# Kernel tuning notes

Measured on AMD Instinct MI355X. Metric: run time of the kernel, lower is better.

The kernel has to match this reference:

```python
import jax, jax.numpy as jnp
import numpy as np

H = 1024      # hidden_size
I = 4096      # intermediate_size
E = 8         # num_experts
TOP_K = 2
LB_COEF = 0.01


def setup_inputs() -> dict:
    key = jax.random.key(0)
    ks = jax.random.split(key, 8)
    s_h = 1.0 / np.sqrt(H)
    s_i = 1.0 / np.sqrt(I)
    return {
        "x": jax.random.normal(ks[0], (2, 2048, H), dtype=jnp.float32),
        "Wr": jax.random.normal(ks[1], (H, E), dtype=jnp.float32) * s_h,
        "br": jnp.zeros((E,), dtype=jnp.float32),
        "W1": jax.random.normal(ks[2], (E, H, I), dtype=jnp.float32) * s_h,
        "b1": jnp.zeros((E, I), dtype=jnp.float32),
        "W2": jax.random.normal(ks[3], (E, I, H), dtype=jnp.float32) * s_i,
        "b2": jnp.zeros((E, H), dtype=jnp.float32),
    }


def _moe_forward(x, Wr, br, W1, b1, W2, b2):
    B, S, Hd = x.shape
    x_flat = x.reshape(-1, Hd)                      # [T, H]
    T = x_flat.shape[0]

    # ---- Router: softmax probs, top-k, renormalize ----
    logits = x_flat @ Wr + br                       # [T, E]
    probs = jax.nn.softmax(logits, axis=-1)         # [T, E]
    topk_w, topk_idx = jax.lax.top_k(probs, TOP_K)  # [T, K]
    topk_w = topk_w / jnp.sum(topk_w, axis=-1, keepdims=True)

    # ---- Load-balance aux loss (switch-style) ----
    onehot = jax.nn.one_hot(topk_idx, E, dtype=x.dtype)   # [T, K, E]
    frac_tokens = onehot.mean(axis=(0, 1))                 # [E]
    frac_probs = probs.mean(axis=0)                        # [E]
    aux_loss = E * jnp.sum(frac_tokens * frac_probs) * LB_COEF

    # combine_weights[t, e] = routing weight of expert e for token t (0 if unselected)
    combine = jnp.sum(topk_w[..., None] * onehot, axis=1)  # [T, E]

    # ---- Experts: dense per-expert FFN, weighted combine ----
    out = jnp.zeros_like(x_flat)
    for e in range(E):
        h = jax.nn.gelu(x_flat @ W1[e] + b1[e])            # [T, I]
        y = h @ W2[e] + b2[e]                              # [T, H]
        out = out + y * combine[:, e:e + 1]
    return out.reshape(B, S, Hd), aux_loss


def reference(x, Wr, br, W1, b1, W2, b2):
    return _moe_forward(x, Wr, br, W1, b1, W2, b2)
```

## Files before the change

### kernel.cpp

```cpp
#include <hip/hip_runtime.h>
#include <hip/hip_bf16.h>

#define HD 1024
#define ID 4096
#define NE 8
#define NT 4096
#define NSLOT (NT*2)

typedef __attribute__((ext_vector_type(4))) float f32x4;
typedef __attribute__((ext_vector_type(8))) short bf16x8;
typedef __attribute__((ext_vector_type(4))) unsigned int u32x4;
typedef __attribute__((ext_vector_type(2))) unsigned int u32x2;
typedef unsigned short u16;

__device__ __forceinline__ u16 f2b(float f) {
  __hip_bfloat16 h = __float2bfloat16(f);
  return __builtin_bit_cast(unsigned short, h);
}
__device__ __forceinline__ unsigned int pack2(float a, float b) {
  return (unsigned int)f2b(a) | ((unsigned int)f2b(b) << 16);
}
__device__ __forceinline__ void gload16(const void* g, void* l) {
  __builtin_amdgcn_global_load_lds(
      (const __attribute__((address_space(1))) unsigned int*)g,
      (__attribute__((address_space(3))) unsigned int*)l, 16, 0, 0);
}
__device__ __forceinline__ float gelu_tanh(float v) {
  float c = v + 0.044715f * v * v * v;
  return 0.5f * v * (1.0f + tanhf(0.7978845608028654f * c));
}

__global__ __launch_bounds__(256) void k_transpose_bf16(
    const float* __restrict__ src, u16* __restrict__ dst, int R, int C) {
  __shared__ float tile[64][65];
  int e = blockIdx.z;
  int c0 = blockIdx.x * 64;
  int r0 = blockIdx.y * 64;
  int t = threadIdx.x;
  const float* s = src + (size_t)e * R * C;
#pragma unroll
  for (int i = 0; i < 16; ++i) {
    int r = i * 4 + (t >> 6);
    tile[r][t & 63] = s[(size_t)(r0 + r) * C + c0 + (t & 63)];
  }
  __syncthreads();
  u16* d = dst + (size_t)e * R * C;
#pragma unroll
  for (int i = 0; i < 4; ++i) {
    int c = i * 16 + (t >> 4);
    int rb = (t & 15) * 4;
    u32x2 p;
    p[0] = pack2(tile[rb + 0][c], tile[rb + 1][c]);
    p[1] = pack2(tile[rb + 2][c], tile[rb + 3][c]);
    *(u32x2*)&d[(size_t)(c0 + c) * R + r0 + rb] = p;
  }
}

__global__ __launch_bounds__(256) void k_router(
    const float* __restrict__ x, const float* __restrict__ Wr,
    const float* __restrict__ br, int* __restrict__ cnt,
    int* __restrict__ slotE, int* __restrict__ slotLoc,
    float* __restrict__ slotW, float* __restrict__ psumG,
    u16* __restrict__ xb) {
  __shared__ float wrt[NE * HD];
  __shared__ float blkp[NE];
  int t = threadIdx.x;
  if (t < NE) blkp[t] = 0.0f;
  for (int i = t; i < NE * HD; i += 256) wrt[(i & 7) * HD + (i >> 3)] = Wr[i];
  __syncthreads();
  int wave = t >> 6, lane = t & 63;
  int token = blockIdx.x * 4 + wave;
  const float* xr = x + (size_t)token * HD;
  u16* xbr = xb + (size_t)token * HD;
  float acc[NE] = {0, 0, 0, 0, 0, 0, 0, 0};
#pragma unroll 4
  for (int j = 0; j < 16; ++j) {
    int h = j * 64 + lane;
    float xv = xr[h];
    xbr[h] = f2b(xv);
#pragma unroll
    for (int e = 0; e < NE; ++e) acc[e] += xv * wrt[e * HD + h];
  }
#pragma unroll
  for (int d = 1; d < 64; d <<= 1) {
#pragma unroll
    for (int e = 0; e < NE; ++e) acc[e] += __shfl_xor(acc[e], d, 64);
  }
  if (lane == 0) {
    float lg[NE], p[NE];
    float m = -1e30f;
#pragma unroll
    for (int e = 0; e < NE; ++e) { lg[e] = acc[e] + br[e]; m = fmaxf(m, lg[e]); }
    float s = 0.f;
#pragma unroll
    for (int e = 0; e < NE; ++e) { p[e] = expf(lg[e] - m); s += p[e]; }
    float inv = 1.0f / s;
    int i1 = 0, i2 = -1;
    float v1 = -1.f, v2 = -1.f;
#pragma unroll
    for (int e = 0; e < NE; ++e) {
      p[e] *= inv;
      atomicAdd(&blkp[e], p[e]);
      if (p[e] > v1) { v2 = v1; i2 = i1; v1 = p[e]; i1 = e; }
      else if (p[e] > v2) { v2 = p[e]; i2 = e; }
    }
    float wsum = v1 + v2;
    int l1 = atomicAdd(&cnt[i1], 1);
    int l2 = atomicAdd(&cnt[i2], 1);
    slotE[token * 2] = i1;     slotLoc[token * 2] = l1;     slotW[token * 2] = v1 / wsum;
    slotE[token * 2 + 1] = i2; slotLoc[token * 2 + 1] = l2; slotW[token * 2 + 1] = v2 / wsum;
  }
  __syncthreads();
  if (t < NE) atomicAdd(&psumG[t], blkp[t]);
}

__global__ void k_finalize(const float* __restrict__ psumG, const int* __restrict__ cnt,
                           int* __restrict__ off, float* __restrict__ out_aux) {
  if (threadIdx.x == 0) {
    int o = 0;
    float a = 0.f;
    for (int e = 0; e < NE; ++e) {
      off[e] = o;
      o += cnt[e];
      a += ((float)cnt[e] / (float)NSLOT) * (psumG[e] / (float)NT);
    }
    off[NE] = o;
    out_aux[0] = (float)NE * a * 0.01f;
  }
}

__global__ void k_scatter(const int* __restrict__ slotE, const int* __restrict__ slotLoc,
                          const float* __restrict__ slotW, const int* __restrict__ off,
                          int* __restrict__ rowTok, float* __restrict__ rowW) {
  int i = blockIdx.x * 256 + threadIdx.x;
  int pos = off[slotE[i]] + slotLoc[i];
  if (pos < 0) pos = 0;
  if (pos >= NSLOT) pos = NSLOT - 1;
  rowTok[pos] = i >> 1;
  rowW[pos] = slotW[i];
}

#define STG(bf) do { \
    gload16(srcA0, &As[bf][c0 * 8]); \
    gload16(srcA1, &As[bf][c1 * 8]); \
    gload16(srcB0, &Bs[bf][c0 * 8]); \
    gload16(srcB1, &Bs[bf][c1 * 8]); \
    srcA0 += 32; srcA1 += 32; srcB0 += 32; srcB1 += 32; \
  } while (0)

__global__ __launch_bounds__(512, 1) void k_gemm1(
    const u16* __restrict__ xb, const u16* __restrict__ w1t,
    const float* __restrict__ b1, u16* __restrict__ hbuf,
    const int* __restrict__ cnt, const int* __restrict__ off,
    const int* __restrict__ rowTok) {
  int bid = blockIdx.x;
  int e = bid >> 8;
  int m0 = ((bid >> 4) & 15) * 256;
  int n0 = (bid & 15) * 256;
  int ce = cnt[e];
  if (m0 >= ce) return;
  int oe = off[e];
  __shared__ u16 As[3][256 * 32];
  __shared__ u16 Bs[3][256 * 32];
  __shared__ int rtok[256];
  int t = threadIdx.x;
  if (t < 256) {
    int r = m0 + t;
    if (r >= ce) r = ce - 1;
    int tok = rowTok[oe + r];
    rtok[t] = (tok < 0) ? 0 : (tok >= NT ? NT - 1 : tok);
  }
  __syncthreads();
  int c0 = t, c1 = t + 512;
  int js0 = (c0 & 3) ^ ((c0 >> 3) & 3);
  int js1 = (c1 & 3) ^ ((c1 >> 3) & 3);
  const u16* srcA0 = xb + (size_t)rtok[c0 >> 2] * HD + js0 * 8;
  const u16* srcA1 = xb + (size_t)rtok[c1 >> 2] * HD + js1 * 8;
  const u16* bb = w1t + (size_t)e * ID * HD + (size_t)n0 * HD;
  const u16* srcB0 = bb + (size_t)(c0 >> 2) * HD + js0 * 8;
  const u16* srcB1 = bb + (size_t)(c1 >> 2) * HD + js1 * 8;
  int lane = t & 63, wave = t >> 6;
  int wr = wave >> 2, wc = wave & 3;
  f32x4 acc[8][4] = {};
  const int NK = HD / 32;
  STG(0);
  STG(1);
  int rb = 0;
  for (int kt = 0; kt < NK; ++kt) {
    if (kt + 1 < NK) asm volatile("s_waitcnt vmcnt(4)" ::: "memory");
    else             asm volatile("s_waitcnt vmcnt(0)" ::: "memory");
    __builtin_amdgcn_s_barrier();
    bf16x8 af[8], bv[4];
#pragma unroll
    for (int mm = 0; mm < 8; ++mm) {
      int ra = wr * 128 + mm * 16 + (lane & 15);
      int slot = (lane >> 4) ^ ((ra >> 1) & 3);
      af[mm] = *(const bf16x8*)&As[rb][ra * 32 + slot * 8];
    }
#pragma unroll
    for (int nn = 0; nn < 4; ++nn) {
      int rbr = wc * 64 + nn * 16 + (lane & 15);
      int slot = (lane >> 4) ^ ((rbr >> 1) & 3);
      bv[nn] = *(const bf16x8*)&Bs[rb][rbr * 32 + slot * 8];
    }
#pragma unroll
    for (int mm = 0; mm < 8; ++mm)
#pragma unroll
      for (int nn = 0; nn < 4; ++nn)
        acc[mm][nn] = __builtin_amdgcn_mfma_f32_16x16x32_bf16(af[mm], bv[nn], acc[mm][nn], 0, 0, 0);
    if (kt + 2 < NK) {
      int sb = rb + 2; if (sb >= 3) sb -= 3;
      STG(sb);
    }
    rb = (rb == 2) ? 0 : rb + 1;
  }
  const float* b1e = b1 + (size_t)e * ID + n0;
#pragma unroll
  for (int nn = 0; nn < 4; ++nn) {
    int col = wc * 64 + nn * 16 + (lane & 15);
    float bias = b1e[col];
#pragma unroll
    for (int mm = 0; mm < 8; ++mm) {
      int lr0 = wr * 128 + mm * 16 + (lane >> 4) * 4;
#pragma unroll
      for (int r = 0; r < 4; ++r) {
        int grow = m0 + lr0 + r;
        if (grow < ce) {
          float v = acc[mm][nn][r] + bias;
          hbuf[(size_t)(oe + grow) * ID + n0 + col] = f2b(gelu_tanh(v));
        }
      }
    }
  }
}

__global__ __launch_bounds__(512, 1) void k_gemm2(
    const u16* __restrict__ hbuf, const u16* __restrict__ w2t,
    const float* __restrict__ b2, float* __restrict__ out,
    const int* __restrict__ cnt, const int* __restrict__ off,
    const int* __restrict__ rowTok, const float* __restrict__ rowW) {
  int bid = blockIdx.x;
  int e = bid >> 7;
  int m0 = ((bid >> 3) & 15) * 256;
  int n0 = ((bid >> 1) & 3) * 256;
  int ks = bid & 1;
  int ce = cnt[e];
  if (m0 >= ce) return;
  int oe = off[e];
  int k0 = ks * (ID / 2);
  __shared__ u16 As[3][256 * 32];
  __shared__ u16 Bs[3][256 * 32];
  __shared__ int rtok[256];
  __shared__ float rw[256];
  int t = threadIdx.x;
  if (t < 256) {
    int r = m0 + t;
    int rc = (r < ce) ? r : ce - 1;
    int tok = rowTok[oe + rc];
    rtok[t] = (tok < 0) ? 0 : (tok >= NT ? NT - 1 : tok);
    rw[t] = (r < ce) ? rowW[oe + r] : 0.0f;
  }
  __syncthreads();
  int c0 = t, c1 = t + 512;
  int js0 = (c0 & 3) ^ ((c0 >> 3) & 3);
  int js1 = (c1 & 3) ^ ((c1 >> 3) & 3);
  int rA0 = m0 + (c0 >> 2); if (rA0 >= ce) rA0 = ce - 1;
  int rA1 = m0 + (c1 >> 2); if (rA1 >= ce) rA1 = ce - 1;
  const u16* srcA0 = hbuf + (size_t)(oe + rA0) * ID + k0 + js0 * 8;
  const u16* srcA1 = hbuf + (size_t)(oe + rA1) * ID + k0 + js1 * 8;
  const u16* bb = w2t + (size_t)e * HD * ID + (size_t)n0 * ID + k0;
  const u16* srcB0 = bb + (size_t)(c0 >> 2) * ID + js0 * 8;
  const u16* srcB1 = bb + (size_t)(c1 >> 2) * ID + js1 * 8;
  int lane = t & 63, wave = t >> 6;
  int wr = wave >> 2, wc = wave & 3;
  f32x4 acc[8][4] = {};
  const int NK = (ID / 2) / 32;
  STG(0);
  STG(1);
  int rb = 0;
  for (int kt = 0; kt < NK; ++kt) {
    if (kt + 1 < NK) asm volatile("s_waitcnt vmcnt(4)" ::: "memory");
    else             asm volatile("s_waitcnt vmcnt(0)" ::: "memory");
    __builtin_amdgcn_s_barrier();
    bf16x8 af[8], bv[4];
#pragma unroll
    for (int mm = 0; mm < 8; ++mm) {
      int ra = wr * 128 + mm * 16 + (lane & 15);
      int slot = (lane >> 4) ^ ((ra >> 1) & 3);
      af[mm] = *(const bf16x8*)&As[rb][ra * 32 + slot * 8];
    }
#pragma unroll
    for (int nn = 0; nn < 4; ++nn) {
      int rbr = wc * 64 + nn * 16 + (lane & 15);
      int slot = (lane >> 4) ^ ((rbr >> 1) & 3);
      bv[nn] = *(const bf16x8*)&Bs[rb][rbr * 32 + slot * 8];
    }
#pragma unroll
    for (int mm = 0; mm < 8; ++mm)
#pragma unroll
      for (int nn = 0; nn < 4; ++nn)
        acc[mm][nn] = __builtin_amdgcn_mfma_f32_16x16x32_bf16(af[mm], bv[nn], acc[mm][nn], 0, 0, 0);
    if (kt + 2 < NK) {
      int sb = rb + 2; if (sb >= 3) sb -= 3;
      STG(sb);
    }
    rb = (rb == 2) ? 0 : rb + 1;
  }
  const float* b2e = b2 + (size_t)e * HD + n0;
#pragma unroll
  for (int nn = 0; nn < 4; ++nn) {
    int col = wc * 64 + nn * 16 + (lane & 15);
    float bias = (ks == 0) ? b2e[col] : 0.0f;
#pragma unroll
    for (int mm = 0; mm < 8; ++mm) {
      int lr0 = wr * 128 + mm * 16 + (lane >> 4) * 4;
#pragma unroll
      for (int r = 0; r < 4; ++r) {
        int lr = lr0 + r;
        int grow = m0 + lr;
        if (grow < ce) {
          float v = (acc[mm][nn][r] + bias) * rw[lr];
          atomicAdd(&out[(size_t)rtok[lr] * HD + n0 + col], v);
        }
      }
    }
  }
}

extern "C" void kernel_launch(void* const* d_in, const int* in_sizes, int n_in,
                              void* d_out, int out_size, void* d_ws, size_t ws_size,
                              hipStream_t stream) {
  const float* x  = (const float*)d_in[0];
  const float* Wr = (const float*)d_in[1];
  const float* br = (const float*)d_in[2];
  const float* W1 = (const float*)d_in[3];
  const float* b1 = (const float*)d_in[4];
  const float* W2 = (const float*)d_in[5];
  const float* b2 = (const float*)d_in[6];
  float* out = (float*)d_out;

  char* ws = (char*)d_ws;
  size_t o = 0;
  auto alloc = [&](size_t bytes) {
    void* p = ws + o;
    o = (o + bytes + 255) & ~(size_t)255;
    return p;
  };
  u16* xb    = (u16*)alloc((size_t)NT * HD * 2);
  u16* w1t   = (u16*)alloc((size_t)NE * ID * HD * 2);
  u16* w2t   = (u16*)alloc((size_t)NE * ID * HD * 2);
  u16* hbuf  = (u16*)alloc((size_t)NSLOT * ID * 2);
  int* cnt     = (int*)alloc(NE * 4);
  float* psumG = (float*)alloc(NE * 4);
  int* off     = (int*)alloc(16 * 4);
  int* slotE   = (int*)alloc(NSLOT * 4);
  int* slotLoc = (int*)alloc(NSLOT * 4);
  float* slotW = (float*)alloc(NSLOT * 4);
  int* rowTok  = (int*)alloc(NSLOT * 4);
  float* rowW  = (float*)alloc(NSLOT * 4);

  if (ws_size < o) return;

  hipMemsetAsync(cnt, 0, NE * 4, stream);
  hipMemsetAsync(psumG, 0, NE * 4, stream);
  hipMemsetAsync(out, 0, (size_t)out_size * 4, stream);
  k_transpose_bf16<<<dim3(ID / 64, HD / 64, NE), 256, 0, stream>>>(W1, w1t, HD, ID);
  k_transpose_bf16<<<dim3(HD / 64, ID / 64, NE), 256, 0, stream>>>(W2, w2t, ID, HD);
  k_router<<<NT / 4, 256, 0, stream>>>(x, Wr, br, cnt, slotE, slotLoc, slotW, psumG, xb);
  k_finalize<<<1, 64, 0, stream>>>(psumG, cnt, off, out + (size_t)NT * HD);
  k_scatter<<<NSLOT / 256, 256, 0, stream>>>(slotE, slotLoc, slotW, off, rowTok, rowW);
  k_gemm1<<<NE * 16 * 16, 512, 0, stream>>>(xb, w1t, b1, hbuf, cnt, off, rowTok);
  k_gemm2<<<NE * 16 * 4 * 2, 512, 0, stream>>>(hbuf, w2t, b2, out, cnt, off, rowTok, rowW);
}
```

Before: 559.8 us.

## Retile expert GEMMs to 128x256 tiles with 256-thread blocks, two per CU

Both grouped expert GEMMs move from 256x256 tiles run by 512 threads to 128x256 tiles run by 256 threads, with launch bounds allowing two blocks per CU. Each wave now computes 64x128 instead of 128x64, and the staging macro issues six async loads per stage instead of four, with the vmcnt wait adjusted to match. The smaller M tile is meant to waste less work on padded rows at the ragged end of each expert's token count and to give more blocks for load balance. In exchange, each loaded B tile is reused across fewer rows, raising weight traffic, and two resident blocks per CU put more pressure on LDS and registers.

```diff
diff --git a/kernel.cpp b/kernel.cpp
--- a/kernel.cpp
+++ b/kernel.cpp
@@ -141,72 +141,78 @@
 }
 
 #define STG(bf) do { \
-    gload16(srcA0, &As[bf][c0 * 8]); \
-    gload16(srcA1, &As[bf][c1 * 8]); \
-    gload16(srcB0, &Bs[bf][c0 * 8]); \
-    gload16(srcB1, &Bs[bf][c1 * 8]); \
-    srcA0 += 32; srcA1 += 32; srcB0 += 32; srcB1 += 32; \
+    gload16(srcA0, &As[bf][cA0 * 8]); \
+    gload16(srcA1, &As[bf][cA1 * 8]); \
+    gload16(srcB0, &Bs[bf][cB0 * 8]); \
+    gload16(srcB1, &Bs[bf][cB1 * 8]); \
+    gload16(srcB2, &Bs[bf][cB2 * 8]); \
+    gload16(srcB3, &Bs[bf][cB3 * 8]); \
+    srcA0 += 32; srcA1 += 32; srcB0 += 32; srcB1 += 32; srcB2 += 32; srcB3 += 32; \
   } while (0)
 
-__global__ __launch_bounds__(512, 1) void k_gemm1(
+__global__ __launch_bounds__(256, 2) void k_gemm1(
     const u16* __restrict__ xb, const u16* __restrict__ w1t,
     const float* __restrict__ b1, u16* __restrict__ hbuf,
     const int* __restrict__ cnt, const int* __restrict__ off,
     const int* __restrict__ rowTok) {
   int bid = blockIdx.x;
-  int e = bid >> 8;
-  int m0 = ((bid >> 4) & 15) * 256;
+  int e = bid >> 9;
+  int m0 = ((bid >> 4) & 31) * 128;
   int n0 = (bid & 15) * 256;
   int ce = cnt[e];
   if (m0 >= ce) return;
   int oe = off[e];
-  __shared__ u16 As[3][256 * 32];
+  __shared__ u16 As[3][128 * 32];
   __shared__ u16 Bs[3][256 * 32];
-  __shared__ int rtok[256];
+  __shared__ int rtok[128];
   int t = threadIdx.x;
-  if (t < 256) {
+  if (t < 128) {
     int r = m0 + t;
     if (r >= ce) r = ce - 1;
     int tok = rowTok[oe + r];
     rtok[t] = (tok < 0) ? 0 : (tok >= NT ? NT - 1 : tok);
   }
   __syncthreads();
-  int c0 = t, c1 = t + 512;
-  int js0 = (c0 & 3) ^ ((c0 >> 3) & 3);
-  int js1 = (c1 & 3) ^ ((c1 >> 3) & 3);
-  const u16* srcA0 = xb + (size_t)rtok[c0 >> 2] * HD + js0 * 8;
-  const u16* srcA1 = xb + (size_t)rtok[c1 >> 2] * HD + js1 * 8;
+  int cA0 = t, cA1 = t + 256;
+  int cB0 = t, cB1 = t + 256, cB2 = t + 512, cB3 = t + 768;
+  int jA0 = (cA0 & 3) ^ ((cA0 >> 3) & 3), jA1 = (cA1 & 3) ^ ((cA1 >> 3) & 3);
+  int jB0 = (cB0 & 3) ^ ((cB0 >> 3) & 3), jB1 = (cB1 & 3) ^ ((cB1 >> 3) & 3);
+  int jB2 = (cB2 & 3) ^ ((cB2 >> 3) & 3), jB3 = (cB3 & 3) ^ ((cB3 >> 3) & 3);
+  const u16* srcA0 = xb + (size_t)rtok[cA0 >> 2] * HD + jA0 * 8;
+  const u16* srcA1 = xb + (size_t)rtok[cA1 >> 2] * HD + jA1 * 8;
   const u16* bb = w1t + (size_t)e * ID * HD + (size_t)n0 * HD;
-  const u16* srcB0 = bb + (size_t)(c0 >> 2) * HD + js0 * 8;
-  const u16* srcB1 = bb + (size_t)(c1 >> 2) * HD + js1 * 8;
+  const u16* srcB0 = bb + (size_t)(cB0 >> 2) * HD + jB0 * 8;
+  const u16* srcB1 = bb + (size_t)(cB1 >> 2) * HD + jB1 * 8;
+  const u16* srcB2 = bb + (size_t)(cB2 >> 2) * HD + jB2 * 8;
+  const u16* srcB3 = bb + (size_t)(cB3 >> 2) * HD + jB3 * 8;
   int lane = t & 63, wave = t >> 6;
-  int wr = wave >> 2, wc = wave & 3;
-  f32x4 acc[8][4] = {};
+  int wr = wave >> 1, wc = wave & 1;
+  f32x4 acc[4][8] = {};
   const int NK = HD / 32;
   STG(0);
   STG(1);
   int rb = 0;
   for (int kt = 0; kt < NK; ++kt) {
-    if (kt + 1 < NK) asm volatile("s_waitcnt vmcnt(4)" ::: "memory");
+    if (kt + 1 < NK) asm volatile("s_waitcnt vmcnt(6)" ::: "memory");
     else             asm volatile("s_waitcnt vmcnt(0)" ::: "memory");
     __builtin_amdgcn_s_barrier();
-    bf16x8 af[8], bv[4];
-#pragma unroll
-    for (int mm = 0; mm < 8; ++mm) {
-      int ra = wr * 128 + mm * 16 + (lane & 15);
+    bf16x8 af[4], bv[8];
+#pragma unroll
+    for (int mm = 0; mm < 4; ++mm) {
+      int ra = wr * 64 + mm * 16 + (lane & 15);
       int slot = (lane >> 4) ^ ((ra >> 1) & 3);
       af[mm] = *(const bf16x8*)&As[rb][ra * 32 + slot * 8];
     }
 #pragma unroll
-    for (int nn = 0; nn < 4; ++nn) {
-      int rbr = wc * 64 + nn * 16 + (lane & 15);
+    for (int nn = 0; nn < 8; ++nn) {
+      int rbr = wc * 128 + nn * 16 + (lane & 15);
       int slot = (lane >> 4) ^ ((rbr >> 1) & 3);
       bv[nn] = *(const bf16x8*)&Bs[rb][rbr * 32 + slot * 8];
     }
 #pragma unroll
-    for (int mm = 0; mm < 8; ++mm)
-#pragma unroll
-      for (int nn = 0; nn < 4; ++nn)
+    for (int mm = 0; mm < 4; ++mm)
+#pragma unroll
+      for (int nn = 0; nn < 8; ++nn)
         acc[mm][nn] = __builtin_amdgcn_mfma_f32_16x16x32_bf16(af[mm], bv[nn], acc[mm][nn], 0, 0, 0);
     if (kt + 2 < NK) {
       int sb = rb + 2; if (sb >= 3) sb -= 3;
@@ -216,12 +222,12 @@
   }
   const float* b1e = b1 + (size_t)e * ID + n0;
 #pragma unroll
-  for (int nn = 0; nn < 4; ++nn) {
-    int col = wc * 64 + nn * 16 + (lane & 15);
+  for (int nn = 0; nn < 8; ++nn) {
+    int col = wc * 128 + nn * 16 + (lane & 15);
     float bias = b1e[col];
 #pragma unroll
-    for (int mm = 0; mm < 8; ++mm) {
-      int lr0 = wr * 128 + mm * 16 + (lane >> 4) * 4;
+    for (int mm = 0; mm < 4; ++mm) {
+      int lr0 = wr * 64 + mm * 16 + (lane >> 4) * 4;
 #pragma unroll
       for (int r = 0; r < 4; ++r) {
         int grow = m0 + lr0 + r;
@@ -234,26 +240,26 @@
   }
 }
 
-__global__ __launch_bounds__(512, 1) void k_gemm2(
+__global__ __launch_bounds__(256, 2) void k_gemm2(
     const u16* __restrict__ hbuf, const u16* __restrict__ w2t,
     const float* __restrict__ b2, float* __restrict__ out,
     const int* __restrict__ cnt, const int* __restrict__ off,
     const int* __restrict__ rowTok, const float* __restrict__ rowW) {
   int bid = blockIdx.x;
-  int e = bid >> 7;
-  int m0 = ((bid >> 3) & 15) * 256;
+  int e = bid >> 8;
+  int m0 = ((bid >> 3) & 31) * 128;
   int n0 = ((bid >> 1) & 3) * 256;
   int ks = bid & 1;
   int ce = cnt[e];
   if (m0 >= ce) return;
   int oe = off[e];
   int k0 = ks * (ID / 2);
-  __shared__ u16 As[3][256 * 32];
+  __shared__ u16 As[3][128 * 32];
   __shared__ u16 Bs[3][256 * 32];
-  __shared__ int rtok[256];
-  __shared__ float rw[256];
+  __shared__ int rtok[128];
+  __shared__ float rw[128];
   int t = threadIdx.x;
-  if (t < 256) {
+  if (t < 128) {
     int r = m0 + t;
     int rc = (r < ce) ? r : ce - 1;
     int tok = rowTok[oe + rc];
@@ -261,44 +267,48 @@
     rw[t] = (r < ce) ? rowW[oe + r] : 0.0f;
   }
   __syncthreads();
-  int c0 = t, c1 = t + 512;
-  int js0 = (c0 & 3) ^ ((c0 >> 3) & 3);
-  int js1 = (c1 & 3) ^ ((c1 >> 3) & 3);
-  int rA0 = m0 + (c0 >> 2); if (rA0 >= ce) rA0 = ce - 1;
-  int rA1 = m0 + (c1 >> 2); if (rA1 >= ce) rA1 = ce - 1;
-  const u16* srcA0 = hbuf + (size_t)(oe + rA0) * ID + k0 + js0 * 8;
-  const u16* srcA1 = hbuf + (size_t)(oe + rA1) * ID + k0 + js1 * 8;
+  int cA0 = t, cA1 = t + 256;
+  int cB0 = t, cB1 = t + 256, cB2 = t + 512, cB3 = t + 768;
+  int jA0 = (cA0 & 3) ^ ((cA0 >> 3) & 3), jA1 = (cA1 & 3) ^ ((cA1 >> 3) & 3);
+  int jB0 = (cB0 & 3) ^ ((cB0 >> 3) & 3), jB1 = (cB1 & 3) ^ ((cB1 >> 3) & 3);
+  int jB2 = (cB2 & 3) ^ ((cB2 >> 3) & 3), jB3 = (cB3 & 3) ^ ((cB3 >> 3) & 3);
+  int rA0 = m0 + (cA0 >> 2); if (rA0 >= ce) rA0 = ce - 1;
+  int rA1 = m0 + (cA1 >> 2); if (rA1 >= ce) rA1 = ce - 1;
+  const u16* srcA0 = hbuf + (size_t)(oe + rA0) * ID + k0 + jA0 * 8;
+  const u16* srcA1 = hbuf + (size_t)(oe + rA1) * ID + k0 + jA1 * 8;
   const u16* bb = w2t + (size_t)e * HD * ID + (size_t)n0 * ID + k0;
-  const u16* srcB0 = bb + (size_t)(c0 >> 2) * ID + js0 * 8;
-  const u16* srcB1 = bb + (size_t)(c1 >> 2) * ID + js1 * 8;
+  const u16* srcB0 = bb + (size_t)(cB0 >> 2) * ID + jB0 * 8;
+  const u16* srcB1 = bb + (size_t)(cB1 >> 2) * ID + jB1 * 8;
+  const u16* srcB2 = bb + (size_t)(cB2 >> 2) * ID + jB2 * 8;
+  const u16* srcB3 = bb + (size_t)(cB3 >> 2) * ID + jB3 * 8;
   int lane = t & 63, wave = t >> 6;
-  int wr = wave >> 2, wc = wave & 3;
-  f32x4 acc[8][4] = {};
+  int wr = wave >> 1, wc = wave & 1;
+  f32x4 acc[4][8] = {};
   const int NK = (ID / 2) / 32;
   STG(0);
   STG(1);
   int rb = 0;
   for (int kt = 0; kt < NK; ++kt) {
-    if (kt + 1 < NK) asm volatile("s_waitcnt vmcnt(4)" ::: "memory");
+    if (kt + 1 < NK) asm volatile("s_waitcnt vmcnt(6)" ::: "memory");
     else             asm volatile("s_waitcnt vmcnt(0)" ::: "memory");
     __builtin_amdgcn_s_barrier();
-    bf16x8 af[8], bv[4];
-#pragma unroll
-    for (int mm = 0; mm < 8; ++mm) {
-      int ra = wr * 128 + mm * 16 + (lane & 15);
+    bf16x8 af[4], bv[8];
+#pragma unroll
+    for (int mm = 0; mm < 4; ++mm) {
+      int ra = wr * 64 + mm * 16 + (lane & 15);
       int slot = (lane >> 4) ^ ((ra >> 1) & 3);
       af[mm] = *(const bf16x8*)&As[rb][ra * 32 + slot * 8];
     }
 #pragma unroll
-    for (int nn = 0; nn < 4; ++nn) {
-      int rbr = wc * 64 + nn * 16 + (lane & 15);
+    for (int nn = 0; nn < 8; ++nn) {
+      int rbr = wc * 128 + nn * 16 + (lane & 15);
       int slot = (lane >> 4) ^ ((rbr >> 1) & 3);
       bv[nn] = *(const bf16x8*)&Bs[rb][rbr * 32 + slot * 8];
     }
 #pragma unroll
-    for (int mm = 0; mm < 8; ++mm)
-#pragma unroll
-      for (int nn = 0; nn < 4; ++nn)
+    for (int mm = 0; mm < 4; ++mm)
+#pragma unroll
+      for (int nn = 0; nn < 8; ++nn)
         acc[mm][nn] = __builtin_amdgcn_mfma_f32_16x16x32_bf16(af[mm], bv[nn], acc[mm][nn], 0, 0, 0);
     if (kt + 2 < NK) {
       int sb = rb + 2; if (sb >= 3) sb -= 3;
@@ -308,12 +318,12 @@
   }
   const float* b2e = b2 + (size_t)e * HD + n0;
 #pragma unroll
-  for (int nn = 0; nn < 4; ++nn) {
-    int col = wc * 64 + nn * 16 + (lane & 15);
+  for (int nn = 0; nn < 8; ++nn) {
+    int col = wc * 128 + nn * 16 + (lane & 15);
     float bias = (ks == 0) ? b2e[col] : 0.0f;
 #pragma unroll
-    for (int mm = 0; mm < 8; ++mm) {
-      int lr0 = wr * 128 + mm * 16 + (lane >> 4) * 4;
+    for (int mm = 0; mm < 4; ++mm) {
+      int lr0 = wr * 64 + mm * 16 + (lane >> 4) * 4;
 #pragma unroll
       for (int r = 0; r < 4; ++r) {
         int lr = lr0 + r;
@@ -369,6 +379,6 @@
   k_router<<<NT / 4, 256, 0, stream>>>(x, Wr, br, cnt, slotE, slotLoc, slotW, psumG, xb);
   k_finalize<<<1, 64, 0, stream>>>(psumG, cnt, off, out + (size_t)NT * HD);
   k_scatter<<<NSLOT / 256, 256, 0, stream>>>(slotE, slotLoc, slotW, off, rowTok, rowW);
-  k_gemm1<<<NE * 16 * 16, 512, 0, stream>>>(xb, w1t, b1, hbuf, cnt, off, rowTok);
-  k_gemm2<<<NE * 16 * 4 * 2, 512, 0, stream>>>(hbuf, w2t, b2, out, cnt, off, rowTok, rowW);
-}
+  k_gemm1<<<NE * 32 * 16, 256, 0, stream>>>(xb, w1t, b1, hbuf, cnt, off, rowTok);
+  k_gemm2<<<NE * 32 * 4 * 2, 256, 0, stream>>>(hbuf, w2t, b2, out, cnt, off, rowTok, rowW);
+}
```

Measured after the change: 582.2 us. 1.04x slower.

## Double-buffer GEMM LDS, split gemm2 K by four, fuse transposes, faster GELU

Applied to the files above, without the earlier changes.

Reduces the GEMM shared-memory pipeline from three to two stages and adds a barrier before refilling the consumed buffer. Splits gemm2's K dimension into four parts instead of two, so more blocks are in flight but more float atomics hit the output. Merges the two weight-transpose launches into one kernel and rewrites tanh-GELU using an exp-based formula. This trades pipeline depth for lower LDS use and extra parallelism, at the cost of extra barriers and atomic traffic.

```diff
diff --git a/kernel.cpp b/kernel.cpp
--- a/kernel.cpp
+++ b/kernel.cpp
@@ -27,15 +27,30 @@
 }
 __device__ __forceinline__ float gelu_tanh(float v) {
   float c = v + 0.044715f * v * v * v;
-  return 0.5f * v * (1.0f + tanhf(0.7978845608028654f * c));
-}
-
-__global__ __launch_bounds__(256) void k_transpose_bf16(
-    const float* __restrict__ src, u16* __restrict__ dst, int R, int C) {
+  float u = 1.5957691216057308f * c;
+  float t = 1.0f - 2.0f / (__expf(u) + 1.0f);
+  return 0.5f * v * (1.0f + t);
+}
+
+__global__ __launch_bounds__(256) void k_transpose2(
+    const float* __restrict__ W1, u16* __restrict__ w1t,
+    const float* __restrict__ W2, u16* __restrict__ w2t) {
   __shared__ float tile[64][65];
-  int e = blockIdx.z;
-  int c0 = blockIdx.x * 64;
-  int r0 = blockIdx.y * 64;
+  int id = blockIdx.x;
+  const float* src;
+  u16* dst;
+  int R, C, e, rem;
+  if (id < 8192) {
+    e = id >> 10; rem = id & 1023;
+    src = W1; dst = w1t; R = HD; C = ID;
+  } else {
+    id -= 8192;
+    e = id >> 10; rem = id & 1023;
+    src = W2; dst = w2t; R = ID; C = HD;
+  }
+  int ctiles = C >> 6;
+  int c0 = (rem % ctiles) * 64;
+  int r0 = (rem / ctiles) * 64;
   int t = threadIdx.x;
   const float* s = src + (size_t)e * R * C;
 #pragma unroll
@@ -141,10 +156,10 @@
 }
 
 #define STG(bf) do { \
-    gload16(srcA0, &As[bf][c0 * 8]); \
-    gload16(srcA1, &As[bf][c1 * 8]); \
-    gload16(srcB0, &Bs[bf][c0 * 8]); \
-    gload16(srcB1, &Bs[bf][c1 * 8]); \
+    gload16(srcA0, &As[bf][cA0 * 8]); \
+    gload16(srcA1, &As[bf][cA1 * 8]); \
+    gload16(srcB0, &Bs[bf][cB0 * 8]); \
+    gload16(srcB1, &Bs[bf][cB1 * 8]); \
     srcA0 += 32; srcA1 += 32; srcB0 += 32; srcB1 += 32; \
   } while (0)
 
@@ -160,8 +175,8 @@
   int ce = cnt[e];
   if (m0 >= ce) return;
   int oe = off[e];
-  __shared__ u16 As[3][256 * 32];
-  __shared__ u16 Bs[3][256 * 32];
+  __shared__ u16 As[2][256 * 32];
+  __shared__ u16 Bs[2][256 * 32];
   __shared__ int rtok[256];
   int t = threadIdx.x;
   if (t < 256) {
@@ -171,37 +186,37 @@
     rtok[t] = (tok < 0) ? 0 : (tok >= NT ? NT - 1 : tok);
   }
   __syncthreads();
-  int c0 = t, c1 = t + 512;
-  int js0 = (c0 & 3) ^ ((c0 >> 3) & 3);
-  int js1 = (c1 & 3) ^ ((c1 >> 3) & 3);
-  const u16* srcA0 = xb + (size_t)rtok[c0 >> 2] * HD + js0 * 8;
-  const u16* srcA1 = xb + (size_t)rtok[c1 >> 2] * HD + js1 * 8;
+  int cA0 = t, cA1 = t + 512;
+  int cB0 = cA0, cB1 = cA1;
+  int jA0 = (cA0 & 3) ^ ((cA0 >> 3) & 3), jA1 = (cA1 & 3) ^ ((cA1 >> 3) & 3);
+  const u16* srcA0 = xb + (size_t)rtok[cA0 >> 2] * HD + jA0 * 8;
+  const u16* srcA1 = xb + (size_t)rtok[cA1 >> 2] * HD + jA1 * 8;
   const u16* bb = w1t + (size_t)e * ID * HD + (size_t)n0 * HD;
-  const u16* srcB0 = bb + (size_t)(c0 >> 2) * HD + js0 * 8;
-  const u16* srcB1 = bb + (size_t)(c1 >> 2) * HD + js1 * 8;
+  const u16* srcB0 = bb + (size_t)(cB0 >> 2) * HD + jA0 * 8;
+  const u16* srcB1 = bb + (size_t)(cB1 >> 2) * HD + jA1 * 8;
   int lane = t & 63, wave = t >> 6;
   int wr = wave >> 2, wc = wave & 3;
   f32x4 acc[8][4] = {};
   const int NK = HD / 32;
   STG(0);
   STG(1);
-  int rb = 0;
   for (int kt = 0; kt < NK; ++kt) {
     if (kt + 1 < NK) asm volatile("s_waitcnt vmcnt(4)" ::: "memory");
     else             asm volatile("s_waitcnt vmcnt(0)" ::: "memory");
     __builtin_amdgcn_s_barrier();
+    int cb = kt & 1;
     bf16x8 af[8], bv[4];
 #pragma unroll
     for (int mm = 0; mm < 8; ++mm) {
       int ra = wr * 128 + mm * 16 + (lane & 15);
       int slot = (lane >> 4) ^ ((ra >> 1) & 3);
-      af[mm] = *(const bf16x8*)&As[rb][ra * 32 + slot * 8];
+      af[mm] = *(const bf16x8*)&As[cb][ra * 32 + slot * 8];
     }
 #pragma unroll
     for (int nn = 0; nn < 4; ++nn) {
       int rbr = wc * 64 + nn * 16 + (lane & 15);
       int slot = (lane >> 4) ^ ((rbr >> 1) & 3);
-      bv[nn] = *(const bf16x8*)&Bs[rb][rbr * 32 + slot * 8];
+      bv[nn] = *(const bf16x8*)&Bs[cb][rbr * 32 + slot * 8];
     }
 #pragma unroll
     for (int mm = 0; mm < 8; ++mm)
@@ -209,10 +224,9 @@
       for (int nn = 0; nn < 4; ++nn)
         acc[mm][nn] = __builtin_amdgcn_mfma_f32_16x16x32_bf16(af[mm], bv[nn], acc[mm][nn], 0, 0, 0);
     if (kt + 2 < NK) {
-      int sb = rb + 2; if (sb >= 3) sb -= 3;
-      STG(sb);
-    }
-    rb = (rb == 2) ? 0 : rb + 1;
+      __builtin_amdgcn_s_barrier();
+      STG(cb);
+    }
   }
   const float* b1e = b1 + (size_t)e * ID + n0;
 #pragma unroll
@@ -240,16 +254,16 @@
     const int* __restrict__ cnt, const int* __restrict__ off,
     const int* __restrict__ rowTok, const float* __restrict__ rowW) {
   int bid = blockIdx.x;
-  int e = bid >> 7;
-  int m0 = ((bid >> 3) & 15) * 256;
-  int n0 = ((bid >> 1) & 3) * 256;
-  int ks = bid & 1;
+  int e = bid >> 8;
+  int m0 = ((bid >> 4) & 15) * 256;
+  int n0 = ((bid >> 2) & 3) * 256;
+  int ks = bid & 3;
   int ce = cnt[e];
   if (m0 >= ce) return;
   int oe = off[e];
-  int k0 = ks * (ID / 2);
-  __shared__ u16 As[3][256 * 32];
-  __shared__ u16 Bs[3][256 * 32];
+  int k0 = ks * (ID / 4);
+  __shared__ u16 As[2][256 * 32];
+  __shared__ u16 Bs[2][256 * 32];
   __shared__ int rtok[256];
   __shared__ float rw[256];
   int t = threadIdx.x;
@@ -261,39 +275,39 @@
     rw[t] = (r < ce) ? rowW[oe + r] : 0.0f;
   }
   __syncthreads();
-  int c0 = t, c1 = t + 512;
-  int js0 = (c0 & 3) ^ ((c0 >> 3) & 3);
-  int js1 = (c1 & 3) ^ ((c1 >> 3) & 3);
-  int rA0 = m0 + (c0 >> 2); if (rA0 >= ce) rA0 = ce - 1;
-  int rA1 = m0 + (c1 >> 2); if (rA1 >= ce) rA1 = ce - 1;
-  const u16* srcA0 = hbuf + (size_t)(oe + rA0) * ID + k0 + js0 * 8;
-  const u16* srcA1 = hbuf + (size_t)(oe + rA1) * ID + k0 + js1 * 8;
+  int cA0 = t, cA1 = t + 512;
+  int cB0 = cA0, cB1 = cA1;
+  int jA0 = (cA0 & 3) ^ ((cA0 >> 3) & 3), jA1 = (cA1 & 3) ^ ((cA1 >> 3) & 3);
+  int rA0 = m0 + (cA0 >> 2); if (rA0 >= ce) rA0 = ce - 1;
+  int rA1 = m0 + (cA1 >> 2); if (rA1 >= ce) rA1 = ce - 1;
+  const u16* srcA0 = hbuf + (size_t)(oe + rA0) * ID + k0 + jA0 * 8;
+  const u16* srcA1 = hbuf + (size_t)(oe + rA1) * ID + k0 + jA1 * 8;
   const u16* bb = w2t + (size_t)e * HD * ID + (size_t)n0 * ID + k0;
-  const u16* srcB0 = bb + (size_t)(c0 >> 2) * ID + js0 * 8;
-  const u16* srcB1 = bb + (size_t)(c1 >> 2) * ID + js1 * 8;
+  const u16* srcB0 = bb + (size_t)(cB0 >> 2) * ID + jA0 * 8;
+  const u16* srcB1 = bb + (size_t)(cB1 >> 2) * ID + jA1 * 8;
   int lane = t & 63, wave = t >> 6;
   int wr = wave >> 2, wc = wave & 3;
   f32x4 acc[8][4] = {};
-  const int NK = (ID / 2) / 32;
+  const int NK = (ID / 4) / 32;
   STG(0);
   STG(1);
-  int rb = 0;
   for (int kt = 0; kt < NK; ++kt) {
     if (kt + 1 < NK) asm volatile("s_waitcnt vmcnt(4)" ::: "memory");
     else             asm volatile("s_waitcnt vmcnt(0)" ::: "memory");
     __builtin_amdgcn_s_barrier();
+    int cb = kt & 1;
     bf16x8 af[8], bv[4];
 #pragma unroll
     for (int mm = 0; mm < 8; ++mm) {
       int ra = wr * 128 + mm * 16 + (lane & 15);
       int slot = (lane >> 4) ^ ((ra >> 1) & 3);
-      af[mm] = *(const bf16x8*)&As[rb][ra * 32 + slot * 8];
+      af[mm] = *(const bf16x8*)&As[cb][ra * 32 + slot * 8];
     }
 #pragma unroll
     for (int nn = 0; nn < 4; ++nn) {
       int rbr = wc * 64 + nn * 16 + (lane & 15);
       int slot = (lane >> 4) ^ ((rbr >> 1) & 3);
-      bv[nn] = *(const bf16x8*)&Bs[rb][rbr * 32 + slot * 8];
+      bv[nn] = *(const bf16x8*)&Bs[cb][rbr * 32 + slot * 8];
     }
 #pragma unroll
     for (int mm = 0; mm < 8; ++mm)
@@ -301,10 +315,9 @@
       for (int nn = 0; nn < 4; ++nn)
         acc[mm][nn] = __builtin_amdgcn_mfma_f32_16x16x32_bf16(af[mm], bv[nn], acc[mm][nn], 0, 0, 0);
     if (kt + 2 < NK) {
-      int sb = rb + 2; if (sb >= 3) sb -= 3;
-      STG(sb);
-    }
-    rb = (rb == 2) ? 0 : rb + 1;
+      __builtin_amdgcn_s_barrier();
+      STG(cb);
+    }
   }
   const float* b2e = b2 + (size_t)e * HD + n0;
 #pragma unroll
@@ -361,14 +374,13 @@
 
   if (ws_size < o) return;
 
-  hipMemsetAsync(cnt, 0, NE * 4, stream);
-  hipMemsetAsync(psumG, 0, NE * 4, stream);
-  hipMemsetAsync(out, 0, (size_t)out_size * 4, stream);
-  k_transpose_bf16<<<dim3(ID / 64, HD / 64, NE), 256, 0, stream>>>(W1, w1t, HD, ID);
-  k_transpose_bf16<<<dim3(HD / 64, ID / 64, NE), 256, 0, stream>>>(W2, w2t, ID, HD);
+  (void)hipMemsetAsync(cnt, 0, NE * 4, stream);
+  (void)hipMemsetAsync(psumG, 0, NE * 4, stream);
+  (void)hipMemsetAsync(out, 0, (size_t)out_size * 4, stream);
+  k_transpose2<<<16384, 256, 0, stream>>>(W1, w1t, W2, w2t);
   k_router<<<NT / 4, 256, 0, stream>>>(x, Wr, br, cnt, slotE, slotLoc, slotW, psumG, xb);
   k_finalize<<<1, 64, 0, stream>>>(psumG, cnt, off, out + (size_t)NT * HD);
   k_scatter<<<NSLOT / 256, 256, 0, stream>>>(slotE, slotLoc, slotW, off, rowTok, rowW);
   k_gemm1<<<NE * 16 * 16, 512, 0, stream>>>(xb, w1t, b1, hbuf, cnt, off, rowTok);
-  k_gemm2<<<NE * 16 * 4 * 2, 512, 0, stream>>>(hbuf, w2t, b2, out, cnt, off, rowTok, rowW);
-}
+  k_gemm2<<<NE * 16 * 4 * 4, 512, 0, stream>>>(hbuf, w2t, b2, out, cnt, off, rowTok, rowW);
+}
```

Measured after the change: 616.0 us. 1.1x slower.
